# Kernel optimization log

Measured on AMD Instinct MI355X. Metric: run time of the kernel, lower is better.

## Reference

```python
import jax, jax.numpy as jnp
import numpy as np

# J2 (von Mises) elastic-plastic material, plane strain, linear isotropic hardening.
# State per integration point: committed strain (3), in-plane stress (3), out-of-plane
# stress szz (1), equivalent plastic strain eqps (1, the 'history' variable).
E_MOD = 3130.0   # Young's modulus (epoxy-like, MPa)
NU = 0.37        # Poisson ratio
SIGY0 = 64.8     # initial yield stress
HARD = 100.0     # linear hardening modulus
G_MOD = E_MOD / (2.0 * (1.0 + NU))
LAM = E_MOD * NU / ((1.0 + NU) * (1.0 - 2.0 * NU))


def _elastic_D():
    c = E_MOD / ((1.0 + NU) * (1.0 - 2.0 * NU))
    return jnp.array([[c * (1.0 - NU), c * NU, 0.0],
                      [c * NU, c * (1.0 - NU), 0.0],
                      [0.0, 0.0, G_MOD]], dtype=jnp.float32)


def _j2_step(carry, strain_t):
    # strain_t: [P,3] total strain (engineering shear) at this timestep
    eps_old, sig_old, szz_old, eqps = carry
    D = _elastic_D()
    deps = strain_t - eps_old
    sig_tr = sig_old + deps @ D.T                       # trial in-plane stress [P,3]
    szz_tr = szz_old + LAM * (deps[:, 0] + deps[:, 1])  # plane-strain out-of-plane stress
    p = (sig_tr[:, 0] + sig_tr[:, 1] + szz_tr) / 3.0
    dxx = sig_tr[:, 0] - p
    dyy = sig_tr[:, 1] - p
    dzz = szz_tr - p
    dxy = sig_tr[:, 2]
    q = jnp.sqrt(1.5 * (dxx * dxx + dyy * dyy + dzz * dzz + 2.0 * dxy * dxy) + 1e-12)
    f = q - (SIGY0 + HARD * eqps)
    dgam = jnp.where(f > 0.0, f / (3.0 * G_MOD + HARD), 0.0)  # radial return
    fac = 1.0 - 3.0 * G_MOD * dgam / q
    sig_new = jnp.stack([p + fac * dxx, p + fac * dyy, fac * dxy], axis=-1)
    szz_new = p + fac * dzz
    eqps_new = eqps + dgam  # commit()
    return (strain_t, sig_new, szz_new, eqps_new), sig_new


def reference(x, W1, W2):
    # x: [B,S,F]; W1: [ls,F] (fc1, no bias); W2: [O,ls] (softLayer: softplus-constrained weights)
    B, S, F = x.shape
    ls = W1.shape[0]
    bulk = ls // 3
    P = B * bulk
    # fc1 for all timesteps at once, then reshape to per-point strains [S, P, 3]
    strains = jnp.einsum('bsf,hf->bsh', x, W1)
    strains = strains.reshape(B, S, bulk, 3).transpose(1, 0, 2, 3).reshape(S, P, 3)
    init = (jnp.zeros((P, 3), jnp.float32), jnp.zeros((P, 3), jnp.float32),
            jnp.zeros((P,), jnp.float32), jnp.zeros((P,), jnp.float32))
    _, stresses = jax.lax.scan(_j2_step, init, strains)        # [S, P, 3]
    stresses = stresses.reshape(S, B, ls).transpose(1, 0, 2)   # [B, S, ls]
    out = jnp.einsum('bsh,oh->bso', stresses, jax.nn.softplus(W2))
    return out


def setup_inputs() -> dict:
    key = jax.random.key(0)
    k1, k2, k3 = jax.random.split(key, 3)
    B, S, F, ls, O = 128, 2048, 3, 192, 3
    x = jax.random.normal(k1, (B, S, F), dtype=jnp.float32) * 0.01  # strain-scale inputs
    W1 = jax.random.normal(k2, (ls, F), dtype=jnp.float32) / np.sqrt(F)
    W2 = jax.random.normal(k3, (O, ls), dtype=jnp.float32) / np.sqrt(ls)
    return {"x": x, "W1": W1, "W2": W2}
```

## Files before the change

### kernel.cpp

```cpp
#include <hip/hip_runtime.h>
#include <cmath>

namespace {
constexpr float kE   = 3130.0f;
constexpr float kNu  = 0.37f;
constexpr float kSy0 = 64.8f;
constexpr float kH   = 100.0f;
constexpr float kG   = kE / (2.0f * (1.0f + kNu));
constexpr float kLam = kE * kNu / ((1.0f + kNu) * (1.0f - 2.0f * kNu));
constexpr float kC   = kE / ((1.0f + kNu) * (1.0f - 2.0f * kNu));
constexpr float kC11 = kC * (1.0f - kNu);
constexpr float kC12 = kC * kNu;
constexpr float kC2  = 3.0f * kG / (3.0f * kG + kH);
constexpr float kC3  = kH / (3.0f * kG + kH);
constexpr int kS  = 2048;
constexpr int kT  = 16;
constexpr int kNBLK = kS / kT;
constexpr int kLs = 192;
constexpr float kSq15  = 1.224744871391589f;
constexpr float kSq3   = 1.732050807568877f;
constexpr float kISq15 = 1.0f / kSq15;
constexpr float kISq3  = 1.0f / kSq3;
}

typedef __fp16 half2_t __attribute__((ext_vector_type(2)));
typedef float f4_t __attribute__((ext_vector_type(4)));

__device__ __forceinline__ unsigned pk16(float a, float b) {
    half2_t h = __builtin_amdgcn_cvt_pkrtz(a, b);
    return __builtin_bit_cast(unsigned, h);
}
__device__ __forceinline__ float up16lo(unsigned u) {
    half2_t h = __builtin_bit_cast(half2_t, u);
    return (float)h.x;
}
__device__ __forceinline__ float up16hi(unsigned u) {
    half2_t h = __builtin_bit_cast(half2_t, u);
    return (float)h.y;
}

template<int CTRL, int RM, int BM>
__device__ __forceinline__ float dppmov(float v) {
    return __int_as_float(
        __builtin_amdgcn_update_dpp(0, __float_as_int(v), CTRL, RM, BM, false));
}
__device__ __forceinline__ float wave_sum63(float v) {
    v += dppmov<0x111, 0xf, 0xf>(v);
    v += dppmov<0x112, 0xf, 0xf>(v);
    v += dppmov<0x114, 0xf, 0xf>(v);
    v += dppmov<0x118, 0xf, 0xf>(v);
    v += dppmov<0x142, 0xa, 0xf>(v);
    v += dppmov<0x143, 0xc, 0xf>(v);
    return v;
}
template<int CTRL>
__device__ __forceinline__ float qdpp(float v) {
    return __int_as_float(
        __builtin_amdgcn_update_dpp(0, __float_as_int(v), CTRL, 0xF, 0xF, true));
}

__device__ __align__(16) float g_dx[128 * 2048 * 3];

__global__ __launch_bounds__(256, 4)
void j2_dx(const float* __restrict__ x)
{
    const int gid = blockIdx.x * 256 + threadIdx.x;
    const int t = gid & 2047;
    const float* xe = x + (size_t)gid * 3;
    const float a0 = xe[0], a1 = xe[1], a2 = xe[2];
    float p0 = 0.f, p1 = 0.f, p2 = 0.f;
    if (t != 0) { p0 = xe[-3]; p1 = xe[-2]; p2 = xe[-1]; }
    float* o = g_dx + (size_t)gid * 3;
    o[0] = a0 - p0; o[1] = a1 - p1; o[2] = a2 - p2;
}

__global__ __launch_bounds__(64, 1)
void j2_scan4(const float* __restrict__ W1, unsigned* __restrict__ ws32)
{
    const int b   = blockIdx.x;
    const int qtr = blockIdx.y;
    const int ln  = threadIdx.x;
    const int kc  = ln >> 2;
    const int c   = ln & 3;
    const int kg  = qtr * 16 + kc;

    float gv[3];
#pragma unroll
    for (int f = 0; f < 3; ++f) {
        const float w0 = W1[(3 * kg + 0) * 3 + f];
        const float w1 = W1[(3 * kg + 1) * 3 + f];
        const float w2 = W1[(3 * kg + 2) * 3 + f];
        const float e0 = kC11 * w0 + kC12 * w1;
        const float e1 = kC12 * w0 + kC11 * w1;
        const float lv = kLam * (w0 + w1);
        const float g0 = kSq15 * (2.0f * e0 - e1 - lv) * (1.0f / 3.0f);
        const float g1 = kSq15 * (2.0f * e1 - e0 - lv) * (1.0f / 3.0f);
        const float g2 = kSq3 * kG * w2;
        const float gz = -(g0 + g1);
        gv[f] = (c == 0) ? g0 : (c == 1) ? g1 : (c == 2) ? g2 : gz;
    }

    const float* db = g_dx + (size_t)b * (kS * 3);
    unsigned* wsb = ws32 + (size_t)b * 1024 * 256 + qtr * 64 + ln;

    float s = 0.f, y = kSy0, c2y = kC2 * kSy0;

    auto loadw = [&](f4_t* dst, int p) {
        const f4_t* s4 = reinterpret_cast<const f4_t*>(db + p * 48);
#pragma unroll
        for (int i = 0; i < 12; ++i) dst[i] = s4[i];
    };

    auto body = [&](const f4_t* Wd, int p) {
        float u[kT];
#pragma unroll
        for (int t = 0; t < kT; ++t) {
            const float d0 = Wd[(3 * t + 0) >> 2][(3 * t + 0) & 3];
            const float d1 = Wd[(3 * t + 1) >> 2][(3 * t + 1) & 3];
            const float d2 = Wd[(3 * t + 2) >> 2][(3 * t + 2) & 3];
            u[t] = fmaf(gv[0], d0, fmaf(gv[1], d1, gv[2] * d2));
        }
        float se = 0.f;
#pragma unroll
        for (int t = 0; t < kT; ++t) {
            const float st = s + u[t];
            float pp = fmaf(st, st, 2.5e-13f);
            pp += qdpp<0xB1>(pp);
            pp += qdpp<0x4E>(pp);
            const float rq  = __builtin_amdgcn_rsqf(pp);
            const float fac = fminf(fmaf(c2y, rq, kC3), 1.0f);
            s = fac * st;
            const float qv = pp * rq;
            y = fmaxf(y, fmaf(kC3, qv, c2y));
            c2y = kC2 * y;
            if ((t & 1) == 0) {
                se = s;
            } else {
                wsb[(size_t)(p * 8 + (t >> 1)) * 256] = pk16(se, s);
            }
        }
    };

    f4_t A[12], B[12];
    loadw(A, 0);
    for (int p = 0; p < kNBLK; p += 2) {
        loadw(B, p + 1);
        body(A, p);
        if (p + 2 < kNBLK) loadw(A, p + 2);
        body(B, p + 1);
    }
}

__global__ __launch_bounds__(64, 1)
void j2_out_einsum(const float* __restrict__ x,
                   const float* __restrict__ W1,
                   const float* __restrict__ W2,
                   const uint4* __restrict__ ws,
                   float* __restrict__ out)
{
    const int b = blockIdx.x;
    const int tile = blockIdx.y;
    const int k = threadIdx.x;

    float wr[3][3];
#pragma unroll
    for (int j = 0; j < 3; ++j)
#pragma unroll
        for (int f = 0; f < 3; ++f)
            wr[j][f] = W1[(3 * k + j) * 3 + f];
    float mv[3];
#pragma unroll
    for (int f = 0; f < 3; ++f) {
        const float e0 = kC11 * wr[0][f] + kC12 * wr[1][f];
        const float e1 = kC12 * wr[0][f] + kC11 * wr[1][f];
        const float lv = kLam * (wr[0][f] + wr[1][f]);
        mv[f] = (e0 + e1 + lv) * (1.0f / 3.0f);
    }
    float spp[3][3], so[3];
#pragma unroll
    for (int o = 0; o < 3; ++o) {
        const float a0 = __logf(1.0f + __expf(W2[o * kLs + 3 * k + 0]));
        const float a1 = __logf(1.0f + __expf(W2[o * kLs + 3 * k + 1]));
        const float a2 = __logf(1.0f + __expf(W2[o * kLs + 3 * k + 2]));
        spp[o][0] = a0 * kISq15;
        spp[o][1] = a1 * kISq15;
        spp[o][2] = a2 * kISq3;
        so[o] = a0 + a1;
    }

    float fx[48];
    {
        const float4* s4 = reinterpret_cast<const float4*>(
            x + (size_t)b * (kS * 3) + tile * 48);
#pragma unroll
        for (int i = 0; i < 12; ++i) {
            float4 v = s4[i];
            fx[4 * i]     = v.x; fx[4 * i + 1] = v.y;
            fx[4 * i + 2] = v.z; fx[4 * i + 3] = v.w;
        }
    }

    float r[48];
#pragma unroll
    for (int j = 0; j < 8; ++j) {
        const uint4 v = ws[((size_t)b * 1024 + tile * 8 + j) * 64 + k];
#pragma unroll
        for (int h = 0; h < 2; ++h) {
            const int t = 2 * j + h;
            const float sx = h ? up16hi(v.x) : up16lo(v.x);
            const float sy = h ? up16hi(v.y) : up16lo(v.y);
            const float sv = h ? up16hi(v.z) : up16lo(v.z);
            const float pm = fmaf(mv[0], fx[3 * t],
                             fmaf(mv[1], fx[3 * t + 1], mv[2] * fx[3 * t + 2]));
#pragma unroll
            for (int o = 0; o < 3; ++o) {
                const float A = fmaf(spp[o][0], sx,
                                fmaf(spp[o][1], sy, spp[o][2] * sv));
                r[3 * t + o] = fmaf(pm, so[o], A);
            }
        }
    }
#pragma unroll
    for (int v = 0; v < 48; ++v) r[v] = wave_sum63(r[v]);
    if (k == 63) {
        float4* o4 = reinterpret_cast<float4*>(
            out + (size_t)b * (kS * 3) + tile * 48);
#pragma unroll
        for (int i = 0; i < 12; ++i)
            o4[i] = make_float4(r[4 * i], r[4 * i + 1],
                                r[4 * i + 2], r[4 * i + 3]);
    }
}

__global__ __launch_bounds__(192, 1)
void j2_pc_kernel(const float* __restrict__ x,
                  const float* __restrict__ W1,
                  const float* __restrict__ W2,
                  float* __restrict__ out)
{
    __shared__ float4 ubuf[2][kT][64];
    __shared__ float4 sgbuf[2][kT][64];

    const int b = blockIdx.x;
    const int w = threadIdx.x >> 6;
    const int k = threadIdx.x & 63;

    const float* xb = x + (size_t)b * (kS * 3);
    float* ob = out + (size_t)b * (kS * 3);

    float e0[3], e1[3], e2[3], lv[3], sp[3][3];
    if (w != 0) {
        float wr[3][3];
#pragma unroll
        for (int j = 0; j < 3; ++j)
#pragma unroll
            for (int f = 0; f < 3; ++f)
                wr[j][f] = W1[(3 * k + j) * 3 + f];
#pragma unroll
        for (int f = 0; f < 3; ++f) {
            e0[f] = kC11 * wr[0][f] + kC12 * wr[1][f];
            e1[f] = kC12 * wr[0][f] + kC11 * wr[1][f];
            e2[f] = kG * wr[2][f];
            lv[f] = kLam * (wr[0][f] + wr[1][f]);
        }
#pragma unroll
        for (int o = 0; o < 3; ++o)
#pragma unroll
            for (int j = 0; j < 3; ++j) {
                float v = W2[o * kLs + 3 * k + j];
                sp[o][j] = log1pf(expf(v));
            }
    }

    float sg0 = 0.f, sg1 = 0.f, sg2 = 0.f, szz = 0.f;
    float y = kSy0;
    const int tlo = (w == 2) ? 8 : 0;
    constexpr float kInv3GH = 1.0f / (3.0f * kG + kH);
    constexpr float k3G = 3.0f * kG;

    for (int phase = 0; phase <= kNBLK + 1; ++phase) {
        if (w == 0) {
            if (phase >= 1 && phase <= kNBLK) {
                const int blk = phase - 1, pb = blk & 1;
                float4 u[kT];
#pragma unroll
                for (int t = 0; t < kT; ++t) u[t] = ubuf[pb][t][k];
#pragma unroll
                for (int t = 0; t < kT; ++t) {
                    const float t0 = sg0 + u[t].x;
                    const float t1 = sg1 + u[t].y;
                    const float t2 = sg2 + u[t].z;
                    const float tz = szz + u[t].w;
                    const float pm  = (t0 + t1 + tz) * (1.0f / 3.0f);
                    const float dxx = t0 - pm, dyy = t1 - pm, dzz = tz - pm;
                    const float sa  = fmaf(dxx, dxx, dyy * dyy);
                    const float sb  = fmaf(dzz, dzz, (2.0f * t2) * t2);
                    const float q2  = fmaf(1.5f, sa + sb, 1e-12f);
                    const float qq  = __builtin_amdgcn_sqrtf(q2);
                    const float rq  = __builtin_amdgcn_rcpf(qq);
                    const float f   = qq - y;
                    const float dg  = (f > 0.0f) ? f * kInv3GH : 0.0f;
                    y = fmaf(kH, dg, y);
                    const float fac = fmaf(-(k3G * dg), rq, 1.0f);
                    sg0 = fmaf(fac, dxx, pm);
                    sg1 = fmaf(fac, dyy, pm);
                    sg2 = fac * t2;
                    szz = fmaf(fac, dzz, pm);
                    sgbuf[pb][t][k] = make_float4(sg0, sg1, sg2, 0.f);
                }
            }
        } else {
            if (phase < kNBLK) {
                const int p = phase, pb = p & 1;
                float xv[28];
                if (w == 1) {
                    if (p == 0) {
                        xv[0] = xv[1] = xv[2] = xv[3] = 0.f;
                        const float4* s4 = reinterpret_cast<const float4*>(xb);
#pragma unroll
                        for (int i = 0; i < 6; ++i) {
                            float4 v = s4[i];
                            xv[4 + 4 * i] = v.x; xv[5 + 4 * i] = v.y;
                            xv[6 + 4 * i] = v.z; xv[7 + 4 * i] = v.w;
                        }
                    } else {
                        const float4* s4 =
                            reinterpret_cast<const float4*>(xb + p * 48 - 4);
#pragma unroll
                        for (int i = 0; i < 7; ++i) {
                            float4 v = s4[i];
                            xv[4 * i]     = v.x; xv[4 * i + 1] = v.y;
                            xv[4 * i + 2] = v.z; xv[4 * i + 3] = v.w;
                        }
                    }
                } else {
                    const float4* s4 =
                        reinterpret_cast<const float4*>(xb + p * 48 + 20);
#pragma unroll
                    for (int i = 0; i < 7; ++i) {
                        float4 v = s4[i];
                        xv[4 * i]     = v.x; xv[4 * i + 1] = v.y;
                        xv[4 * i + 2] = v.z; xv[4 * i + 3] = v.w;
                    }
                }
                const int tbase = (w == 2) ? 8 : 0;
#pragma unroll
                for (int t = 0; t < 8; ++t) {
                    const float dx0 = xv[3 * t + 4] - xv[3 * t + 1];
                    const float dx1 = xv[3 * t + 5] - xv[3 * t + 2];
                    const float dx2 = xv[3 * t + 6] - xv[3 * t + 3];
                    float4 u;
                    u.x = fmaf(e0[0], dx0, fmaf(e0[1], dx1, e0[2] * dx2));
                    u.y = fmaf(e1[0], dx0, fmaf(e1[1], dx1, e1[2] * dx2));
                    u.z = fmaf(e2[0], dx0, fmaf(e2[1], dx1, e2[2] * dx2));
                    u.w = fmaf(lv[0], dx0, fmaf(lv[1], dx1, lv[2] * dx2));
                    ubuf[pb][tbase + t][k] = u;
                }
            }
            if (phase >= 2) {
                const int q = phase - 2, qb = q & 1;
                const int tbase = tlo;
                float r[24];
#pragma unroll
                for (int t = 0; t < 8; ++t) {
                    float4 s = sgbuf[qb][tbase + t][k];
                    r[3 * t]     = fmaf(sp[0][0], s.x, fmaf(sp[0][1], s.y, sp[0][2] * s.z));
                    r[3 * t + 1] = fmaf(sp[1][0], s.x, fmaf(sp[1][1], s.y, sp[1][2] * s.z));
                    r[3 * t + 2] = fmaf(sp[2][0], s.x, fmaf(sp[2][1], s.y, sp[2][2] * s.z));
                }
#pragma unroll
                for (int v = 0; v < 24; ++v) r[v] = wave_sum63(r[v]);
                if (k == 63) {
                    float4* o4 = reinterpret_cast<float4*>(ob + q * 48 + tbase * 3);
#pragma unroll
                    for (int i = 0; i < 6; ++i)
                        o4[i] = make_float4(r[4 * i], r[4 * i + 1],
                                            r[4 * i + 2], r[4 * i + 3]);
                }
            }
        }
        __syncthreads();
    }
}

extern "C" void kernel_launch(void* const* d_in, const int* in_sizes, int n_in,
                              void* d_out, int out_size, void* d_ws, size_t ws_size,
                              hipStream_t stream) {
    const float* x  = (const float*)d_in[0];
    const float* W1 = (const float*)d_in[1];
    const float* W2 = (const float*)d_in[2];
    float* out = (float*)d_out;

    const size_t need = (size_t)128 * 1024 * 64 * sizeof(uint4);
    if (ws_size >= need) {
        j2_dx<<<dim3(1024), dim3(256), 0, stream>>>(x);
        j2_scan4<<<dim3(128, 4), dim3(64), 0, stream>>>(W1, (unsigned*)d_ws);
        j2_out_einsum<<<dim3(128, 128), dim3(64), 0, stream>>>(
            x, W1, W2, (const uint4*)d_ws, out);
    } else {
        j2_pc_kernel<<<dim3(128), dim3(192), 0, stream>>>(x, W1, W2, out);
    }
}
```

Baseline: 150.1 us.

## Fuse scan and output projection via LDS producer-consumer, reduce partials separately

The separate output-einsum kernel is replaced by two consumer waves inside the scan block. They read the fp16-packed stresses from a double-buffered LDS slot each 16-step tile, synchronised with __syncthreads. Each consumer writes one of 8 partial outputs per (quarter, half) to a workspace, and a small final kernel sums them. This removes the large global round-trip of per-point stresses (about 64 MB of workspace) and the cross-lane reductions. In exchange it adds a block barrier per tile on the serial scan's critical path, plus 8x partial-output traffic.

```diff
diff --git a/kernel.cpp b/kernel.cpp
--- a/kernel.cpp
+++ b/kernel.cpp
@@ -21,6 +21,7 @@
 constexpr float kSq3   = 1.732050807568877f;
 constexpr float kISq15 = 1.0f / kSq15;
 constexpr float kISq3  = 1.0f / kSq3;
+constexpr int kPartStride = 128 * 2048 * 3;
 }
 
 typedef __fp16 half2_t __attribute__((ext_vector_type(2)));
@@ -57,6 +58,10 @@
 __device__ __forceinline__ float qdpp(float v) {
     return __int_as_float(
         __builtin_amdgcn_update_dpp(0, __float_as_int(v), CTRL, 0xF, 0xF, true));
+}
+
+__device__ __forceinline__ float softplusf(float v) {
+    return log1pf(expf(v));
 }
 
 __device__ __align__(16) float g_dx[128 * 2048 * 3];
@@ -74,162 +79,162 @@
     o[0] = a0 - p0; o[1] = a1 - p1; o[2] = a2 - p2;
 }
 
-__global__ __launch_bounds__(64, 1)
-void j2_scan4(const float* __restrict__ W1, unsigned* __restrict__ ws32)
+__global__ __launch_bounds__(192, 1)
+void j2_fused(const float* __restrict__ x,
+              const float* __restrict__ W1,
+              const float* __restrict__ W2,
+              float* __restrict__ partials)
 {
+    __shared__ unsigned sg[2][64 * 8];
+
     const int b   = blockIdx.x;
     const int qtr = blockIdx.y;
-    const int ln  = threadIdx.x;
-    const int kc  = ln >> 2;
-    const int c   = ln & 3;
-    const int kg  = qtr * 16 + kc;
-
-    float gv[3];
-#pragma unroll
-    for (int f = 0; f < 3; ++f) {
-        const float w0 = W1[(3 * kg + 0) * 3 + f];
-        const float w1 = W1[(3 * kg + 1) * 3 + f];
-        const float w2 = W1[(3 * kg + 2) * 3 + f];
-        const float e0 = kC11 * w0 + kC12 * w1;
-        const float e1 = kC12 * w0 + kC11 * w1;
-        const float lv = kLam * (w0 + w1);
-        const float g0 = kSq15 * (2.0f * e0 - e1 - lv) * (1.0f / 3.0f);
-        const float g1 = kSq15 * (2.0f * e1 - e0 - lv) * (1.0f / 3.0f);
-        const float g2 = kSq3 * kG * w2;
-        const float gz = -(g0 + g1);
-        gv[f] = (c == 0) ? g0 : (c == 1) ? g1 : (c == 2) ? g2 : gz;
+    const int w   = threadIdx.x >> 6;
+    const int ln  = threadIdx.x & 63;
+
+    if (w == 0) {
+        const int kc = ln >> 2;
+        const int c  = ln & 3;
+        const int kg = qtr * 16 + kc;
+
+        float gv[3];
+#pragma unroll
+        for (int f = 0; f < 3; ++f) {
+            const float w0 = W1[(3 * kg + 0) * 3 + f];
+            const float w1 = W1[(3 * kg + 1) * 3 + f];
+            const float w2 = W1[(3 * kg + 2) * 3 + f];
+            const float e0 = kC11 * w0 + kC12 * w1;
+            const float e1 = kC12 * w0 + kC11 * w1;
+            const float lv = kLam * (w0 + w1);
+            const float g0 = kSq15 * (2.0f * e0 - e1 - lv) * (1.0f / 3.0f);
+            const float g1 = kSq15 * (2.0f * e1 - e0 - lv) * (1.0f / 3.0f);
+            const float g2 = kSq3 * kG * w2;
+            const float gz = -(g0 + g1);
+            gv[f] = (c == 0) ? g0 : (c == 1) ? g1 : (c == 2) ? g2 : gz;
+        }
+
+        const float* db = g_dx + (size_t)b * (kS * 3);
+        float s = 0.f, y = kSy0, c2y = kC2 * kSy0;
+
+        auto loadw = [&](f4_t* dst, int p) {
+            const f4_t* s4 = reinterpret_cast<const f4_t*>(db + p * 48);
+#pragma unroll
+            for (int i = 0; i < 12; ++i) dst[i] = s4[i];
+        };
+
+        auto body = [&](const f4_t* Wd, int p) {
+            float u[kT];
+#pragma unroll
+            for (int t = 0; t < kT; ++t) {
+                const float d0 = Wd[(3 * t + 0) >> 2][(3 * t + 0) & 3];
+                const float d1 = Wd[(3 * t + 1) >> 2][(3 * t + 1) & 3];
+                const float d2 = Wd[(3 * t + 2) >> 2][(3 * t + 2) & 3];
+                u[t] = fmaf(gv[0], d0, fmaf(gv[1], d1, gv[2] * d2));
+            }
+            unsigned* dstb = &sg[p & 1][ln * 8];
+            float se = 0.f;
+#pragma unroll
+            for (int t = 0; t < kT; ++t) {
+                const float st = s + u[t];
+                float pp = fmaf(st, st, 2.5e-13f);
+                pp += qdpp<0xB1>(pp);
+                pp += qdpp<0x4E>(pp);
+                const float rq  = __builtin_amdgcn_rsqf(pp);
+                const float fac = fminf(fmaf(c2y, rq, kC3), 1.0f);
+                s = fac * st;
+                const float qv = pp * rq;
+                y = fmaxf(y, fmaf(kC3, qv, c2y));
+                c2y = kC2 * y;
+                if ((t & 1) == 0) se = s;
+                else              dstb[t >> 1] = pk16(se, s);
+            }
+        };
+
+        f4_t A[12], B[12];
+        loadw(A, 0);
+        for (int p = 0; p <= kNBLK; ++p) {
+            if (p < kNBLK) {
+                if (p + 1 < kNBLK) {
+                    if (p & 1) loadw(A, p + 1); else loadw(B, p + 1);
+                }
+                body((p & 1) ? B : A, p);
+            }
+            __syncthreads();
+        }
+    } else {
+        const int half = w - 1;
+        const bool act = (ln < 48);
+        const int t  = act ? (ln / 3) : 15;
+        const int o  = act ? (ln % 3) : 0;
+        const int t2 = t >> 1, th = t & 1;
+        const int kcl0 = half * 8;
+        const int kg0  = qtr * 16 + kcl0;
+
+        float spp[8][3], Mv0 = 0.f, Mv1 = 0.f, Mv2 = 0.f;
+#pragma unroll
+        for (int j = 0; j < 8; ++j) {
+            const int kg = kg0 + j;
+            const float a0 = softplusf(W2[o * kLs + 3 * kg + 0]);
+            const float a1 = softplusf(W2[o * kLs + 3 * kg + 1]);
+            const float a2 = softplusf(W2[o * kLs + 3 * kg + 2]);
+            spp[j][0] = a0 * kISq15;
+            spp[j][1] = a1 * kISq15;
+            spp[j][2] = a2 * kISq3;
+            const float so = a0 + a1;
+#pragma unroll
+            for (int f = 0; f < 3; ++f) {
+                const float w0 = W1[(3 * kg + 0) * 3 + f];
+                const float w1 = W1[(3 * kg + 1) * 3 + f];
+                const float e0 = kC11 * w0 + kC12 * w1;
+                const float e1 = kC12 * w0 + kC11 * w1;
+                const float lv = kLam * (w0 + w1);
+                const float mv = (e0 + e1 + lv) * (1.0f / 3.0f);
+                const float c_ = so * mv;
+                if (f == 0) Mv0 += c_;
+                else if (f == 1) Mv1 += c_;
+                else Mv2 += c_;
+            }
+        }
+
+        const float* xb = x + (size_t)b * (kS * 3);
+        float* pout = partials + (size_t)(qtr * 2 + half) * kPartStride
+                      + (size_t)b * (kS * 3);
+
+        for (int p = 0; p <= kNBLK; ++p) {
+            __syncthreads();
+            if (p >= kNBLK) break;
+            const int tabs = p * kT + t;
+            const float x0 = xb[tabs * 3 + 0];
+            const float x1 = xb[tabs * 3 + 1];
+            const float x2 = xb[tabs * 3 + 2];
+            float r = fmaf(Mv0, x0, fmaf(Mv1, x1, Mv2 * x2));
+            const unsigned* sb = &sg[p & 1][0];
+#pragma unroll
+            for (int j = 0; j < 8; ++j) {
+                const int base = ((kcl0 + j) * 4) * 8 + t2;
+                const unsigned u0 = sb[base];
+                const unsigned u1 = sb[base + 8];
+                const unsigned u2 = sb[base + 16];
+                const float s0 = th ? up16hi(u0) : up16lo(u0);
+                const float s1 = th ? up16hi(u1) : up16lo(u1);
+                const float s2 = th ? up16hi(u2) : up16lo(u2);
+                r = fmaf(spp[j][0], s0,
+                    fmaf(spp[j][1], s1, fmaf(spp[j][2], s2, r)));
+            }
+            if (act) pout[tabs * 3 + o] = r;
+        }
     }
-
-    const float* db = g_dx + (size_t)b * (kS * 3);
-    unsigned* wsb = ws32 + (size_t)b * 1024 * 256 + qtr * 64 + ln;
-
-    float s = 0.f, y = kSy0, c2y = kC2 * kSy0;
-
-    auto loadw = [&](f4_t* dst, int p) {
-        const f4_t* s4 = reinterpret_cast<const f4_t*>(db + p * 48);
-#pragma unroll
-        for (int i = 0; i < 12; ++i) dst[i] = s4[i];
-    };
-
-    auto body = [&](const f4_t* Wd, int p) {
-        float u[kT];
-#pragma unroll
-        for (int t = 0; t < kT; ++t) {
-            const float d0 = Wd[(3 * t + 0) >> 2][(3 * t + 0) & 3];
-            const float d1 = Wd[(3 * t + 1) >> 2][(3 * t + 1) & 3];
-            const float d2 = Wd[(3 * t + 2) >> 2][(3 * t + 2) & 3];
-            u[t] = fmaf(gv[0], d0, fmaf(gv[1], d1, gv[2] * d2));
-        }
-        float se = 0.f;
-#pragma unroll
-        for (int t = 0; t < kT; ++t) {
-            const float st = s + u[t];
-            float pp = fmaf(st, st, 2.5e-13f);
-            pp += qdpp<0xB1>(pp);
-            pp += qdpp<0x4E>(pp);
-            const float rq  = __builtin_amdgcn_rsqf(pp);
-            const float fac = fminf(fmaf(c2y, rq, kC3), 1.0f);
-            s = fac * st;
-            const float qv = pp * rq;
-            y = fmaxf(y, fmaf(kC3, qv, c2y));
-            c2y = kC2 * y;
-            if ((t & 1) == 0) {
-                se = s;
-            } else {
-                wsb[(size_t)(p * 8 + (t >> 1)) * 256] = pk16(se, s);
-            }
-        }
-    };
-
-    f4_t A[12], B[12];
-    loadw(A, 0);
-    for (int p = 0; p < kNBLK; p += 2) {
-        loadw(B, p + 1);
-        body(A, p);
-        if (p + 2 < kNBLK) loadw(A, p + 2);
-        body(B, p + 1);
-    }
-}
-
-__global__ __launch_bounds__(64, 1)
-void j2_out_einsum(const float* __restrict__ x,
-                   const float* __restrict__ W1,
-                   const float* __restrict__ W2,
-                   const uint4* __restrict__ ws,
-                   float* __restrict__ out)
+}
+
+__global__ __launch_bounds__(256, 4)
+void j2_final(const float* __restrict__ partials, float* __restrict__ out)
 {
-    const int b = blockIdx.x;
-    const int tile = blockIdx.y;
-    const int k = threadIdx.x;
-
-    float wr[3][3];
-#pragma unroll
-    for (int j = 0; j < 3; ++j)
-#pragma unroll
-        for (int f = 0; f < 3; ++f)
-            wr[j][f] = W1[(3 * k + j) * 3 + f];
-    float mv[3];
-#pragma unroll
-    for (int f = 0; f < 3; ++f) {
-        const float e0 = kC11 * wr[0][f] + kC12 * wr[1][f];
-        const float e1 = kC12 * wr[0][f] + kC11 * wr[1][f];
-        const float lv = kLam * (wr[0][f] + wr[1][f]);
-        mv[f] = (e0 + e1 + lv) * (1.0f / 3.0f);
-    }
-    float spp[3][3], so[3];
-#pragma unroll
-    for (int o = 0; o < 3; ++o) {
-        const float a0 = __logf(1.0f + __expf(W2[o * kLs + 3 * k + 0]));
-        const float a1 = __logf(1.0f + __expf(W2[o * kLs + 3 * k + 1]));
-        const float a2 = __logf(1.0f + __expf(W2[o * kLs + 3 * k + 2]));
-        spp[o][0] = a0 * kISq15;
-        spp[o][1] = a1 * kISq15;
-        spp[o][2] = a2 * kISq3;
-        so[o] = a0 + a1;
-    }
-
-    float fx[48];
-    {
-        const float4* s4 = reinterpret_cast<const float4*>(
-            x + (size_t)b * (kS * 3) + tile * 48);
-#pragma unroll
-        for (int i = 0; i < 12; ++i) {
-            float4 v = s4[i];
-            fx[4 * i]     = v.x; fx[4 * i + 1] = v.y;
-            fx[4 * i + 2] = v.z; fx[4 * i + 3] = v.w;
-        }
-    }
-
-    float r[48];
-#pragma unroll
-    for (int j = 0; j < 8; ++j) {
-        const uint4 v = ws[((size_t)b * 1024 + tile * 8 + j) * 64 + k];
-#pragma unroll
-        for (int h = 0; h < 2; ++h) {
-            const int t = 2 * j + h;
-            const float sx = h ? up16hi(v.x) : up16lo(v.x);
-            const float sy = h ? up16hi(v.y) : up16lo(v.y);
-            const float sv = h ? up16hi(v.z) : up16lo(v.z);
-            const float pm = fmaf(mv[0], fx[3 * t],
-                             fmaf(mv[1], fx[3 * t + 1], mv[2] * fx[3 * t + 2]));
-#pragma unroll
-            for (int o = 0; o < 3; ++o) {
-                const float A = fmaf(spp[o][0], sx,
-                                fmaf(spp[o][1], sy, spp[o][2] * sv));
-                r[3 * t + o] = fmaf(pm, so[o], A);
-            }
-        }
-    }
-#pragma unroll
-    for (int v = 0; v < 48; ++v) r[v] = wave_sum63(r[v]);
-    if (k == 63) {
-        float4* o4 = reinterpret_cast<float4*>(
-            out + (size_t)b * (kS * 3) + tile * 48);
-#pragma unroll
-        for (int i = 0; i < 12; ++i)
-            o4[i] = make_float4(r[4 * i], r[4 * i + 1],
-                                r[4 * i + 2], r[4 * i + 3]);
-    }
+    const int gid = blockIdx.x * 256 + threadIdx.x;
+    float acc = partials[gid];
+#pragma unroll
+    for (int h = 1; h < 8; ++h)
+        acc += partials[(size_t)h * kPartStride + gid];
+    out[gid] = acc;
 }
 
 __global__ __launch_bounds__(192, 1)
@@ -391,12 +396,12 @@
     const float* W2 = (const float*)d_in[2];
     float* out = (float*)d_out;
 
-    const size_t need = (size_t)128 * 1024 * 64 * sizeof(uint4);
+    const size_t need = (size_t)8 * kPartStride * sizeof(float);
     if (ws_size >= need) {
+        float* partials = (float*)d_ws;
         j2_dx<<<dim3(1024), dim3(256), 0, stream>>>(x);
-        j2_scan4<<<dim3(128, 4), dim3(64), 0, stream>>>(W1, (unsigned*)d_ws);
-        j2_out_einsum<<<dim3(128, 128), dim3(64), 0, stream>>>(
-            x, W1, W2, (const uint4*)d_ws, out);
+        j2_fused<<<dim3(128, 4), dim3(192), 0, stream>>>(x, W1, W2, partials);
+        j2_final<<<dim3(3072), dim3(256), 0, stream>>>(partials, out);
     } else {
         j2_pc_kernel<<<dim3(128), dim3(192), 0, stream>>>(x, W1, W2, out);
     }
```

After: 207.1 us. 1.38x slower.

## Merge four scan quarter-blocks into one block with interleaved recurrences

Applied to the files above, without the earlier changes.

Each thread now runs four independent J2 state recurrences (one per former quarter) interleaved in the inner time loop, and launches 128 blocks instead of 128x4. The goal is to hide the latency of the serial reduction/rsqrt chain with instruction-level parallelism and to load the strain increments once per batch instead of four times. In exchange, fewer wavefronts occupy the GPU and register pressure per thread grows.

```diff
diff --git a/kernel.cpp b/kernel.cpp
--- a/kernel.cpp
+++ b/kernel.cpp
@@ -75,35 +75,39 @@
 }
 
 __global__ __launch_bounds__(64, 1)
-void j2_scan4(const float* __restrict__ W1, unsigned* __restrict__ ws32)
+void j2_scan16(const float* __restrict__ W1, unsigned* __restrict__ ws32)
 {
-    const int b   = blockIdx.x;
-    const int qtr = blockIdx.y;
-    const int ln  = threadIdx.x;
-    const int kc  = ln >> 2;
-    const int c   = ln & 3;
-    const int kg  = qtr * 16 + kc;
-
-    float gv[3];
-#pragma unroll
-    for (int f = 0; f < 3; ++f) {
-        const float w0 = W1[(3 * kg + 0) * 3 + f];
-        const float w1 = W1[(3 * kg + 1) * 3 + f];
-        const float w2 = W1[(3 * kg + 2) * 3 + f];
-        const float e0 = kC11 * w0 + kC12 * w1;
-        const float e1 = kC12 * w0 + kC11 * w1;
-        const float lv = kLam * (w0 + w1);
-        const float g0 = kSq15 * (2.0f * e0 - e1 - lv) * (1.0f / 3.0f);
-        const float g1 = kSq15 * (2.0f * e1 - e0 - lv) * (1.0f / 3.0f);
-        const float g2 = kSq3 * kG * w2;
-        const float gz = -(g0 + g1);
-        gv[f] = (c == 0) ? g0 : (c == 1) ? g1 : (c == 2) ? g2 : gz;
+    const int b  = blockIdx.x;
+    const int ln = threadIdx.x;
+    const int kc = ln >> 2;
+    const int c  = ln & 3;
+
+    float gv[4][3];
+#pragma unroll
+    for (int X = 0; X < 4; ++X) {
+        const int kg = 16 * X + kc;
+#pragma unroll
+        for (int f = 0; f < 3; ++f) {
+            const float w0 = W1[(3 * kg + 0) * 3 + f];
+            const float w1 = W1[(3 * kg + 1) * 3 + f];
+            const float w2 = W1[(3 * kg + 2) * 3 + f];
+            const float e0 = kC11 * w0 + kC12 * w1;
+            const float e1 = kC12 * w0 + kC11 * w1;
+            const float lv = kLam * (w0 + w1);
+            const float g0 = kSq15 * (2.0f * e0 - e1 - lv) * (1.0f / 3.0f);
+            const float g1 = kSq15 * (2.0f * e1 - e0 - lv) * (1.0f / 3.0f);
+            const float g2 = kSq3 * kG * w2;
+            const float gz = -(g0 + g1);
+            gv[X][f] = (c == 0) ? g0 : (c == 1) ? g1 : (c == 2) ? g2 : gz;
+        }
     }
 
     const float* db = g_dx + (size_t)b * (kS * 3);
-    unsigned* wsb = ws32 + (size_t)b * 1024 * 256 + qtr * 64 + ln;
-
-    float s = 0.f, y = kSy0, c2y = kC2 * kSy0;
+    unsigned* wsb = ws32 + (size_t)b * (1024 * 256) + ln;
+
+    float s[4], y[4], c2y[4];
+#pragma unroll
+    for (int X = 0; X < 4; ++X) { s[X] = 0.f; y[X] = kSy0; c2y[X] = kC2 * kSy0; }
 
     auto loadw = [&](f4_t* dst, int p) {
         const f4_t* s4 = reinterpret_cast<const f4_t*>(db + p * 48);
@@ -112,31 +116,33 @@
     };
 
     auto body = [&](const f4_t* Wd, int p) {
-        float u[kT];
+        float se[4];
 #pragma unroll
         for (int t = 0; t < kT; ++t) {
             const float d0 = Wd[(3 * t + 0) >> 2][(3 * t + 0) & 3];
             const float d1 = Wd[(3 * t + 1) >> 2][(3 * t + 1) & 3];
             const float d2 = Wd[(3 * t + 2) >> 2][(3 * t + 2) & 3];
-            u[t] = fmaf(gv[0], d0, fmaf(gv[1], d1, gv[2] * d2));
-        }
-        float se = 0.f;
-#pragma unroll
-        for (int t = 0; t < kT; ++t) {
-            const float st = s + u[t];
-            float pp = fmaf(st, st, 2.5e-13f);
-            pp += qdpp<0xB1>(pp);
-            pp += qdpp<0x4E>(pp);
-            const float rq  = __builtin_amdgcn_rsqf(pp);
-            const float fac = fminf(fmaf(c2y, rq, kC3), 1.0f);
-            s = fac * st;
-            const float qv = pp * rq;
-            y = fmaxf(y, fmaf(kC3, qv, c2y));
-            c2y = kC2 * y;
-            if ((t & 1) == 0) {
-                se = s;
-            } else {
-                wsb[(size_t)(p * 8 + (t >> 1)) * 256] = pk16(se, s);
+#pragma unroll
+            for (int X = 0; X < 4; ++X) {
+                const float u  = fmaf(gv[X][0], d0,
+                                 fmaf(gv[X][1], d1, gv[X][2] * d2));
+                const float st = s[X] + u;
+                float pp = fmaf(st, st, 2.5e-13f);
+                pp += qdpp<0xB1>(pp);
+                pp += qdpp<0x4E>(pp);
+                const float rq  = __builtin_amdgcn_rsqf(pp);
+                const float fac = fminf(fmaf(c2y[X], rq, kC3), 1.0f);
+                s[X] = fac * st;
+                const float qv = pp * rq;
+                y[X] = fmaxf(y[X], fmaf(kC3, qv, c2y[X]));
+                c2y[X] = kC2 * y[X];
+                if ((t & 1) == 0) se[X] = s[X];
+            }
+            if (t & 1) {
+                const size_t o = (size_t)(p * 8 + (t >> 1)) * 256;
+#pragma unroll
+                for (int X = 0; X < 4; ++X)
+                    wsb[o + X * 64] = pk16(se[X], s[X]);
             }
         }
     };
@@ -394,7 +400,7 @@
     const size_t need = (size_t)128 * 1024 * 64 * sizeof(uint4);
     if (ws_size >= need) {
         j2_dx<<<dim3(1024), dim3(256), 0, stream>>>(x);
-        j2_scan4<<<dim3(128, 4), dim3(64), 0, stream>>>(W1, (unsigned*)d_ws);
+        j2_scan16<<<dim3(128), dim3(64), 0, stream>>>(W1, (unsigned*)d_ws);
         j2_out_einsum<<<dim3(128, 128), dim3(64), 0, stream>>>(
             x, W1, W2, (const uint4*)d_ws, out);
     } else {
```

New measurement: 339.7 us. +126.3%, slower.

## Map two deviatoric components per lane in J2 scan, halving block count

Applied to the files above, without the earlier changes.

The scan kernel now gives each lane two of the four deviatoric stress components, so one integration point spans two lanes instead of four. This halves the number of wavefronts (256 blocks instead of 512). It replaces one of the two cross-lane DPP reductions with a local FMA, and the stores become one packed uint2 per lane. The serial dependency chain per timestep gets shorter, at the cost of less parallelism across the GPU and more registers per lane.

```diff
diff --git a/kernel.cpp b/kernel.cpp
--- a/kernel.cpp
+++ b/kernel.cpp
@@ -75,16 +75,16 @@
 }
 
 __global__ __launch_bounds__(64, 1)
-void j2_scan4(const float* __restrict__ W1, unsigned* __restrict__ ws32)
+void j2_scan2l(const float* __restrict__ W1, uint2* __restrict__ ws2)
 {
-    const int b   = blockIdx.x;
-    const int qtr = blockIdx.y;
-    const int ln  = threadIdx.x;
-    const int kc  = ln >> 2;
-    const int c   = ln & 3;
-    const int kg  = qtr * 16 + kc;
-
-    float gv[3];
+    const int b    = blockIdx.x >> 1;
+    const int half = blockIdx.x & 1;
+    const int ln   = threadIdx.x;
+    const int kc   = ln >> 1;
+    const int c2   = ln & 1;
+    const int kg   = half * 32 + kc;
+
+    float ga[3], gb[3];
 #pragma unroll
     for (int f = 0; f < 3; ++f) {
         const float w0 = W1[(3 * kg + 0) * 3 + f];
@@ -97,13 +97,15 @@
         const float g1 = kSq15 * (2.0f * e1 - e0 - lv) * (1.0f / 3.0f);
         const float g2 = kSq3 * kG * w2;
         const float gz = -(g0 + g1);
-        gv[f] = (c == 0) ? g0 : (c == 1) ? g1 : (c == 2) ? g2 : gz;
-    }
+        ga[f] = c2 ? g2 : g0;
+        gb[f] = c2 ? gz : g1;
+    }
+    const float eps = c2 ? 0.0f : 1e-12f;
 
     const float* db = g_dx + (size_t)b * (kS * 3);
-    unsigned* wsb = ws32 + (size_t)b * 1024 * 256 + qtr * 64 + ln;
-
-    float s = 0.f, y = kSy0, c2y = kC2 * kSy0;
+    uint2* wsb = ws2 + (size_t)b * (1024 * 128) + kg * 2 + c2;
+
+    float sA = 0.f, sB = 0.f, y = kSy0, c2y = kC2 * kSy0;
 
     auto loadw = [&](f4_t* dst, int p) {
         const f4_t* s4 = reinterpret_cast<const f4_t*>(db + p * 48);
@@ -112,31 +114,31 @@
     };
 
     auto body = [&](const f4_t* Wd, int p) {
-        float u[kT];
+        float seA = 0.f, seB = 0.f;
 #pragma unroll
         for (int t = 0; t < kT; ++t) {
             const float d0 = Wd[(3 * t + 0) >> 2][(3 * t + 0) & 3];
             const float d1 = Wd[(3 * t + 1) >> 2][(3 * t + 1) & 3];
             const float d2 = Wd[(3 * t + 2) >> 2][(3 * t + 2) & 3];
-            u[t] = fmaf(gv[0], d0, fmaf(gv[1], d1, gv[2] * d2));
-        }
-        float se = 0.f;
-#pragma unroll
-        for (int t = 0; t < kT; ++t) {
-            const float st = s + u[t];
-            float pp = fmaf(st, st, 2.5e-13f);
+            const float uA = fmaf(ga[0], d0, fmaf(ga[1], d1, ga[2] * d2));
+            const float uB = fmaf(gb[0], d0, fmaf(gb[1], d1, gb[2] * d2));
+            const float stA = sA + uA;
+            const float stB = sB + uB;
+            float pp = fmaf(stA, stA, eps);
+            pp = fmaf(stB, stB, pp);
             pp += qdpp<0xB1>(pp);
-            pp += qdpp<0x4E>(pp);
             const float rq  = __builtin_amdgcn_rsqf(pp);
             const float fac = fminf(fmaf(c2y, rq, kC3), 1.0f);
-            s = fac * st;
+            sA = fac * stA;
+            sB = fac * stB;
             const float qv = pp * rq;
             y = fmaxf(y, fmaf(kC3, qv, c2y));
             c2y = kC2 * y;
             if ((t & 1) == 0) {
-                se = s;
+                seA = sA; seB = sB;
             } else {
-                wsb[(size_t)(p * 8 + (t >> 1)) * 256] = pk16(se, s);
+                wsb[(size_t)(p * 8 + (t >> 1)) * 128] =
+                    make_uint2(pk16(seA, sA), pk16(seB, sB));
             }
         }
     };
@@ -394,7 +396,7 @@
     const size_t need = (size_t)128 * 1024 * 64 * sizeof(uint4);
     if (ws_size >= need) {
         j2_dx<<<dim3(1024), dim3(256), 0, stream>>>(x);
-        j2_scan4<<<dim3(128, 4), dim3(64), 0, stream>>>(W1, (unsigned*)d_ws);
+        j2_scan2l<<<dim3(256), dim3(64), 0, stream>>>(W1, (uint2*)d_ws);
         j2_out_einsum<<<dim3(128, 128), dim3(64), 0, stream>>>(
             x, W1, W2, (const uint4*)d_ws, out);
     } else {
```

Result: slower. 168.4 us (+12.2%).
